# Kernel tuning notes

Hardware: AMD Instinct MI355X
Metric: run time of the kernel (lower is better)

## Reference

```python
import jax, jax.numpy as jnp
import numpy as np

EPS = 1e-12  # F.normalize default eps

def _l1_normalize(x, axis):
    return x / jnp.maximum(jnp.sum(jnp.abs(x), axis=axis, keepdims=True), EPS)


def setup_inputs() -> dict:
    key = jax.random.key(0)
    k1, k2, k3, k4 = jax.random.split(key, 4)
    B_src, S_src, d = 4096, 32, 512
    B_tgt, T = 32, 256
    m = jax.random.normal(k1, (B_src, S_src, d), dtype=jnp.float32)
    om = jax.random.normal(k2, (B_tgt, T, d), dtype=jnp.float32)
    src_mask = jax.random.randint(k3, (B_src, 1, S_src), 0, 2, dtype=jnp.int32)
    tgt_mask = jax.random.randint(k4, (B_tgt, T, T), 0, 2, dtype=jnp.int32)
    return {"m": m, "om": om, "src_mask": src_mask, "tgt_mask": tgt_mask}


def reference(m, om, src_mask, tgt_mask):
    # masked mean readouts (L1-normalized masks as attention weights)
    src_w = _l1_normalize(src_mask.astype(jnp.float32), axis=-1)      # [B_src,1,S_src]
    src_readout = jnp.einsum('bos,bsd->bod', src_w, m)[:, 0, :]       # [B_src,d]
    tgt_w = _l1_normalize(tgt_mask.astype(jnp.float32), axis=-1)      # [B_tgt,T,T]
    tgt_readout = jnp.einsum('btu,bud->btd', tgt_w, om)               # [B_tgt,T,d]

    # pairwise L2 distance over d WITHOUT materializing [B_tgt,T,B_src,d]:
    # ||t - s||^2 = ||t||^2 + ||s||^2 - 2 t.s
    t_sq = jnp.sum(tgt_readout * tgt_readout, axis=-1)                # [B_tgt,T]
    s_sq = jnp.sum(src_readout * src_readout, axis=-1)                # [B_src]
    cross = jnp.einsum('btd,nd->btn', tgt_readout, src_readout)       # [B_tgt,T,B_src]
    d2 = t_sq[..., None] + s_sq[None, None, :] - 2.0 * cross
    dist = jnp.sqrt(jnp.maximum(d2, EPS))
    sim = jnp.exp(-dist)
    sim = _l1_normalize(sim, axis=-1)                                 # [B_tgt,T,B_src]
    return sim
```

## Files before the change

kernel.cpp:

```cpp
#include <hip/hip_runtime.h>
#include <math.h>

#define EPSF 1e-12f

typedef short bf16x8 __attribute__((ext_vector_type(8)));
typedef float f32x4 __attribute__((ext_vector_type(4)));

__device__ __forceinline__ void gload_lds16(const void* g, void* l) {
  __builtin_amdgcn_global_load_lds(
      (const __attribute__((address_space(1))) unsigned int*)g,
      (__attribute__((address_space(3))) unsigned int*)l, 16, 0, 0);
}

__device__ __forceinline__ unsigned short bf16_rne(float f) {
  unsigned int u = __float_as_uint(f);
  u += 0x7fffu + ((u >> 16) & 1u);
  return (unsigned short)(u >> 16);
}

__device__ __forceinline__ float bf16_to_f32(unsigned short h) {
  return __uint_as_float((unsigned int)h << 16);
}

__device__ __forceinline__ float block_reduce_sum_256(float v) {
#pragma unroll
  for (int o = 32; o > 0; o >>= 1) v += __shfl_down(v, o, 64);
  __shared__ float ws4[4];
  const int lane = threadIdx.x & 63;
  const int w = threadIdx.x >> 6;
  if (lane == 0) ws4[w] = v;
  __syncthreads();
  if (threadIdx.x == 0) ws4[0] = ws4[0] + ws4[1] + ws4[2] + ws4[3];
  __syncthreads();
  return ws4[0];
}

__global__ __launch_bounds__(256) void k_src_readout(const float* __restrict__ m,
                                                     const int* __restrict__ src_mask,
                                                     unsigned short* __restrict__ srcRb,
                                                     float* __restrict__ ssq) {
  const int tid = threadIdx.x;
  const int sub = tid >> 7, t = tid & 127;
  const int b = blockIdx.x * 2 + sub;
  __shared__ int msk[2][32];
  __shared__ float sinv[2];
  __shared__ float red[4];
  if (t < 32) msk[sub][t] = src_mask[b * 32 + t];
  __syncthreads();
  if (t == 0) {
    float c = 0.f;
    for (int s = 0; s < 32; ++s) c += (float)msk[sub][s];
    sinv[sub] = 1.0f / fmaxf(c, EPSF);
  }
  __syncthreads();
  const float inv = sinv[sub];
  const float4* mb = (const float4*)(m + (size_t)b * (32 * 512)) + t;
  float ax = 0.f, ay = 0.f, az = 0.f, aw = 0.f;
  for (int s = 0; s < 32; ++s) {
    if (msk[sub][s] != 0) {
      float4 v = mb[s * 128];
      ax += v.x; ay += v.y; az += v.z; aw += v.w;
    }
  }
  ushort4 o;
  o.x = bf16_rne(ax * inv);
  o.y = bf16_rne(ay * inv);
  o.z = bf16_rne(az * inv);
  o.w = bf16_rne(aw * inv);
  *(ushort4*)(srcRb + (size_t)b * 512 + t * 4) = o;
  float fx = bf16_to_f32(o.x), fy = bf16_to_f32(o.y);
  float fz = bf16_to_f32(o.z), fw = bf16_to_f32(o.w);
  float s = fx * fx + fy * fy + fz * fz + fw * fw;
#pragma unroll
  for (int oo = 32; oo > 0; oo >>= 1) s += __shfl_down(s, oo, 64);
  if ((tid & 63) == 0) red[tid >> 6] = s;
  __syncthreads();
  if (t == 0) ssq[b] = red[sub * 2] + red[sub * 2 + 1];
}

#define WST 72
__global__ __launch_bounds__(512) void k_tgt_readout_mfma(
    const float* __restrict__ om, const int* __restrict__ tgt_mask,
    unsigned short* __restrict__ Afrag) {
  const int b = blockIdx.x, dq = blockIdx.y, th = blockIdx.z;
  const int d0 = dq * 128, t0 = th * 128;
  __shared__ unsigned short Wb[128 * WST];
  __shared__ unsigned short omT[128 * WST];
  __shared__ float cntp[128 * 4];
  __shared__ float cnt_inv[128];
  const int tid = threadIdx.x;
  const int lane = tid & 63, w = tid >> 6;
  const int* mbase = tgt_mask + (size_t)b * 65536 + (size_t)t0 * 256;

  {
    const int t = tid >> 2, q = tid & 3;
    const int* mp = mbase + t * 256 + q * 64;
    int c = 0;
#pragma unroll
    for (int k = 0; k < 16; ++k) {
      int4 v = *(const int4*)(mp + 4 * k);
      c += v.x + v.y + v.z + v.w;
    }
    cntp[t * 4 + q] = (float)c;
  }
  __syncthreads();
  if (tid < 128) {
    float c = cntp[tid * 4] + cntp[tid * 4 + 1] + cntp[tid * 4 + 2] + cntp[tid * 4 + 3];
    cnt_inv[tid] = 1.0f / fmaxf(c, EPSF);
  }

  f32x4 acc[8];
#pragma unroll
  for (int di = 0; di < 8; ++di) acc[di] = (f32x4){0.f, 0.f, 0.f, 0.f};

  for (int uc = 0; uc < 4; ++uc) {
    const int ub = uc * 64;
    __syncthreads();
    {
      const int t = tid >> 2, ul0 = (tid & 3) * 16;
      const int* mp = mbase + t * 256 + ub + ul0;
      unsigned short* wp = Wb + t * WST + ul0;
#pragma unroll
      for (int k = 0; k < 4; ++k) {
        int4 v = *(const int4*)(mp + 4 * k);
        ushort4 h;
        h.x = v.x ? 0x3F80 : 0;
        h.y = v.y ? 0x3F80 : 0;
        h.z = v.z ? 0x3F80 : 0;
        h.w = v.w ? 0x3F80 : 0;
        *(ushort4*)(wp + 4 * k) = h;
      }
    }
    {
#pragma unroll
      for (int k = 0; k < 4; ++k) {
        const int idx = tid + 512 * k;
        const int u = idx >> 5, dl = (idx & 31) * 4;
        float4 v = *(const float4*)(om + (size_t)b * 131072 + (size_t)(ub + u) * 512 + d0 + dl);
        omT[(dl + 0) * WST + u] = bf16_rne(v.x);
        omT[(dl + 1) * WST + u] = bf16_rne(v.y);
        omT[(dl + 2) * WST + u] = bf16_rne(v.z);
        omT[(dl + 3) * WST + u] = bf16_rne(v.w);
      }
    }
    __syncthreads();
#pragma unroll
    for (int kt2 = 0; kt2 < 2; ++kt2) {
      const int ko = kt2 * 32 + (lane >> 4) * 8;
      bf16x8 wf = *(const bf16x8*)(Wb + (w * 16 + (lane & 15)) * WST + ko);
      bf16x8 of[8];
#pragma unroll
      for (int di = 0; di < 8; ++di)
        of[di] = *(const bf16x8*)(omT + (di * 16 + (lane & 15)) * WST + ko);
#pragma unroll
      for (int di = 0; di < 8; ++di)
        acc[di] = __builtin_amdgcn_mfma_f32_16x16x32_bf16(of[di], wf, acc[di], 0, 0, 0);
    }
  }

  const int tl = w * 16 + (lane & 15);
  const int rT = b * 256 + t0 + tl;
  const float inv = cnt_inv[tl];
#pragma unroll
  for (int di = 0; di < 8; ++di) {
    const int d = d0 + di * 16 + (lane >> 4) * 4;
    ushort4 o;
    o.x = bf16_rne(acc[di][0] * inv);
    o.y = bf16_rne(acc[di][1] * inv);
    o.z = bf16_rne(acc[di][2] * inv);
    o.w = bf16_rne(acc[di][3] * inv);
    const size_t off =
        (((size_t)(rT >> 4) * 16 + (d >> 5)) * 64 + ((d >> 3) & 3) * 16 + (rT & 15)) * 8 + (d & 7);
    *(ushort4*)(Afrag + off) = o;
  }
}

__global__ __launch_bounds__(256) void k_rowsq_frag(const unsigned short* __restrict__ Afrag,
                                                    float* __restrict__ sq) {
  const int r = blockIdx.x;
  const int tid = threadIdx.x;
  const int g = r >> 4, rl = r & 15;
  const int d = 2 * tid;
  const size_t off = ((size_t)((g * 16 + (d >> 5)) * 64 + ((d >> 3) & 3) * 16 + rl)) * 8 + (d & 7);
  ushort2 v = *(const ushort2*)(Afrag + off);
  float fx = bf16_to_f32(v.x), fy = bf16_to_f32(v.y);
  float s = fx * fx + fy * fy;
  s = block_reduce_sum_256(s);
  if (tid == 0) sq[r] = s;
}

__global__ __launch_bounds__(512, 2) void k_cross_mfma(
    const unsigned short* __restrict__ Afrag, const unsigned short* __restrict__ B,
    const float* __restrict__ tsq, const float* __restrict__ ssq,
    float* __restrict__ out) {
  __shared__ unsigned short Bs[128 * 512];
  const int tid = threadIdx.x;
  const int lane = tid & 63, w = tid >> 6;
  const int bid = blockIdx.x;
  const int xcd = bid & 7, idx = bid >> 3;
  const int row0 = (xcd * 2 + (idx >> 5)) * 512;
  const int col0 = (idx & 31) * 128;
  const int lr = lane & 15, lkh = lane >> 4;

#pragma unroll
  for (int t = 0; t < 16; ++t) {
    const int c = w * 16 + t;
    const int j = c >> 4, kt = c & 15;
    gload_lds16(B + (size_t)(col0 + j * 16 + lr) * 512 + kt * 32 + lkh * 8,
                Bs + (size_t)c * 512);
  }

  f32x4 acc[4][8];
#pragma unroll
  for (int i = 0; i < 4; ++i)
#pragma unroll
    for (int j = 0; j < 8; ++j) acc[i][j] = (f32x4){0.f, 0.f, 0.f, 0.f};

  __syncthreads();

  const unsigned short* ap = Afrag + ((size_t)(row0 >> 4) + w * 4) * (16 * 64 * 8);
#pragma unroll
  for (int kt = 0; kt < 16; ++kt) {
    bf16x8 af[4], bfr[8];
#pragma unroll
    for (int i = 0; i < 4; ++i)
      af[i] = *(const bf16x8*)(ap + (((size_t)i * 16 + kt) * 64 + lane) * 8);
#pragma unroll
    for (int j = 0; j < 8; ++j)
      bfr[j] = *(const bf16x8*)(Bs + ((j * 16 + kt) * 64 + lane) * 8);
#pragma unroll
    for (int i = 0; i < 4; ++i)
#pragma unroll
      for (int j = 0; j < 8; ++j)
        acc[i][j] = __builtin_amdgcn_mfma_f32_16x16x32_bf16(af[i], bfr[j], acc[i][j], 0, 0, 0);
  }

  const int cbase = col0 + (lane & 15);
  const int rbase = row0 + w * 64 + (lane >> 4) * 4;
  float ss[8];
#pragma unroll
  for (int j = 0; j < 8; ++j) ss[j] = ssq[cbase + j * 16];
#pragma unroll
  for (int i = 0; i < 4; ++i) {
#pragma unroll
    for (int r = 0; r < 4; ++r) {
      const int row = rbase + i * 16 + r;
      const float t2 = tsq[row];
      float* op = out + (size_t)row * 4096 + cbase;
#pragma unroll
      for (int j = 0; j < 8; ++j) {
        float d2 = t2 + ss[j] - 2.0f * acc[i][j][r];
        __builtin_nontemporal_store(expf(-sqrtf(fmaxf(d2, EPSF))), op + j * 16);
      }
    }
  }
}

__global__ __launch_bounds__(256) void k_norm(float* __restrict__ out) {
  const size_t base = (size_t)blockIdx.x * 4096;
  const int tid = threadIdx.x;
  float4 v[4];
  float s = 0.f;
#pragma unroll
  for (int i = 0; i < 4; ++i) {
    v[i] = *(const float4*)(out + base + (size_t)(tid * 4 + i * 1024));
    s += v[i].x + v[i].y + v[i].z + v[i].w;
  }
  s = block_reduce_sum_256(s);
  const float inv = 1.0f / fmaxf(s, EPSF);
#pragma unroll
  for (int i = 0; i < 4; ++i) {
    f32x4 r;
    r[0] = v[i].x * inv;
    r[1] = v[i].y * inv;
    r[2] = v[i].z * inv;
    r[3] = v[i].w * inv;
    __builtin_nontemporal_store(r, (f32x4*)(out + base + (size_t)(tid * 4 + i * 1024)));
  }
}

extern "C" void kernel_launch(void* const* d_in, const int* in_sizes, int n_in,
                              void* d_out, int out_size, void* d_ws, size_t ws_size,
                              hipStream_t stream) {
  const float* m = (const float*)d_in[0];
  const float* om = (const float*)d_in[1];
  const int* src_mask = (const int*)d_in[2];
  const int* tgt_mask = (const int*)d_in[3];
  float* out = (float*)d_out;

  float* ws = (float*)d_ws;
  float* ssq = ws;
  float* tsq = ssq + 4096;
  unsigned short* srcRb = (unsigned short*)(tsq + 8192);
  unsigned short* Afrag = srcRb + 4096 * 512;

  k_src_readout<<<2048, 256, 0, stream>>>(m, src_mask, srcRb, ssq);
  k_tgt_readout_mfma<<<dim3(32, 4, 2), 512, 0, stream>>>(om, tgt_mask, Afrag);
  k_rowsq_frag<<<8192, 256, 0, stream>>>(Afrag, tsq);
  k_cross_mfma<<<512, 512, 0, stream>>>(Afrag, srcRb, tsq, ssq, out);
  k_norm<<<8192, 256, 0, stream>>>(out);
}
```

Measured before the change: 165.2 us.

## Recompute cross GEMM twice to fold L1 normalization into the output write

```diff
diff --git a/kernel.cpp b/kernel.cpp
--- a/kernel.cpp
+++ b/kernel.cpp
@@ -189,9 +189,11 @@
   if (tid == 0) sq[r] = s;
 }
 
-__global__ __launch_bounds__(512, 2) void k_cross_mfma(
+template <int PASS>
+__global__ __launch_bounds__(512, 2) void k_cross_pass(
     const unsigned short* __restrict__ Afrag, const unsigned short* __restrict__ B,
     const float* __restrict__ tsq, const float* __restrict__ ssq,
+    float* __restrict__ psum, const float* __restrict__ rsinv,
     float* __restrict__ out) {
   __shared__ unsigned short Bs[128 * 512];
   const int tid = threadIdx.x;
@@ -246,37 +248,38 @@
     for (int r = 0; r < 4; ++r) {
       const int row = rbase + i * 16 + r;
       const float t2 = tsq[row];
-      float* op = out + (size_t)row * 4096 + cbase;
-#pragma unroll
-      for (int j = 0; j < 8; ++j) {
-        float d2 = t2 + ss[j] - 2.0f * acc[i][j][r];
-        __builtin_nontemporal_store(expf(-sqrtf(fmaxf(d2, EPSF))), op + j * 16);
+      if (PASS == 0) {
+        float s = 0.f;
+#pragma unroll
+        for (int j = 0; j < 8; ++j) {
+          float d2 = t2 + ss[j] - 2.0f * acc[i][j][r];
+          s += expf(-sqrtf(fmaxf(d2, EPSF)));
+        }
+        s += __shfl_xor(s, 1, 64);
+        s += __shfl_xor(s, 2, 64);
+        s += __shfl_xor(s, 4, 64);
+        s += __shfl_xor(s, 8, 64);
+        if ((lane & 15) == 0) psum[(size_t)(col0 >> 7) * 8192 + row] = s;
+      } else {
+        const float rsv = rsinv[row];
+        float* op = out + (size_t)row * 4096 + cbase;
+#pragma unroll
+        for (int j = 0; j < 8; ++j) {
+          float d2 = t2 + ss[j] - 2.0f * acc[i][j][r];
+          __builtin_nontemporal_store(expf(-sqrtf(fmaxf(d2, EPSF))) * rsv, op + j * 16);
+        }
       }
     }
   }
 }
 
-__global__ __launch_bounds__(256) void k_norm(float* __restrict__ out) {
-  const size_t base = (size_t)blockIdx.x * 4096;
-  const int tid = threadIdx.x;
-  float4 v[4];
+__global__ __launch_bounds__(256) void k_sum_reduce(const float* __restrict__ psum,
+                                                    float* __restrict__ rsinv) {
+  const int row = blockIdx.x * 256 + threadIdx.x;
   float s = 0.f;
 #pragma unroll
-  for (int i = 0; i < 4; ++i) {
-    v[i] = *(const float4*)(out + base + (size_t)(tid * 4 + i * 1024));
-    s += v[i].x + v[i].y + v[i].z + v[i].w;
-  }
-  s = block_reduce_sum_256(s);
-  const float inv = 1.0f / fmaxf(s, EPSF);
-#pragma unroll
-  for (int i = 0; i < 4; ++i) {
-    f32x4 r;
-    r[0] = v[i].x * inv;
-    r[1] = v[i].y * inv;
-    r[2] = v[i].z * inv;
-    r[3] = v[i].w * inv;
-    __builtin_nontemporal_store(r, (f32x4*)(out + base + (size_t)(tid * 4 + i * 1024)));
-  }
+  for (int ct = 0; ct < 32; ++ct) s += psum[(size_t)ct * 8192 + row];
+  rsinv[row] = 1.0f / fmaxf(s, EPSF);
 }
 
 extern "C" void kernel_launch(void* const* d_in, const int* in_sizes, int n_in,
@@ -291,12 +294,15 @@
   float* ws = (float*)d_ws;
   float* ssq = ws;
   float* tsq = ssq + 4096;
-  unsigned short* srcRb = (unsigned short*)(tsq + 8192);
+  float* rsinv = tsq + 8192;
+  float* psum = rsinv + 8192;
+  unsigned short* srcRb = (unsigned short*)(psum + 32 * 8192);
   unsigned short* Afrag = srcRb + 4096 * 512;
 
   k_src_readout<<<2048, 256, 0, stream>>>(m, src_mask, srcRb, ssq);
   k_tgt_readout_mfma<<<dim3(32, 4, 2), 512, 0, stream>>>(om, tgt_mask, Afrag);
   k_rowsq_frag<<<8192, 256, 0, stream>>>(Afrag, tsq);
-  k_cross_mfma<<<512, 512, 0, stream>>>(Afrag, srcRb, tsq, ssq, out);
-  k_norm<<<8192, 256, 0, stream>>>(out);
-}
+  k_cross_pass<0><<<512, 512, 0, stream>>>(Afrag, srcRb, tsq, ssq, psum, rsinv, out);
+  k_sum_reduce<<<32, 256, 0, stream>>>(psum, rsinv);
+  k_cross_pass<1><<<512, 512, 0, stream>>>(Afrag, srcRb, tsq, ssq, psum, rsinv, out);
+}
```

After: 202.2 us. +22.4%, slower.
